# Kernel optimization log

Hardware: AMD Instinct MI355X
Metric: run time of the kernel (lower is better)

The kernel has to match this reference:

```python
import jax, jax.numpy as jnp
import numpy as np


def setup_inputs() -> dict:
    key = jax.random.key(0)
    k1, k2, k3, k4 = jax.random.split(key, 4)
    B, S, D, U = 4, 2048, 512, 256
    x = jax.random.normal(k1, (B, S, D), dtype=jnp.float32)
    scale = 1.0 / np.sqrt(D)  # ~glorot magnitude
    Wq = jax.random.normal(k2, (D, U), dtype=jnp.float32) * scale
    Wk = jax.random.normal(k3, (D, U), dtype=jnp.float32) * scale
    Wv = jax.random.normal(k4, (D, U), dtype=jnp.float32) * scale
    return {"x": x, "Wq": Wq, "Wk": Wk, "Wv": Wv}


def reference(x, Wq, Wk, Wv):
    # Single-head self-attention, NO 1/sqrt(d) scaling (faithful to source).
    q = jnp.einsum("bsd,du->bsu", x, Wq)
    k = jnp.einsum("bsd,du->bsu", x, Wk)
    v = jnp.einsum("bsd,du->bsu", x, Wv)
    scores = jnp.einsum("bsu,btu->bst", q, k)       # [B,S,S]
    attn = jax.nn.softmax(scores, axis=-1)
    out = jnp.einsum("bst,btu->bsu", attn, v)       # [B,S,U]
    return out
```

## Files before the change

kernel.cpp:

```cpp
#include <hip/hip_runtime.h>
#include <hip/hip_bf16.h>

typedef _Float16 f16;
typedef _Float16 f16x8 __attribute__((ext_vector_type(8)));
typedef _Float16 f16x4 __attribute__((ext_vector_type(4)));
typedef float    f32x4 __attribute__((ext_vector_type(4)));

#define DEV __device__ __forceinline__

DEV f16x8 load16(const void* p) {
  return __builtin_bit_cast(f16x8, *(const uint4*)p);
}
DEV f32x4 mfma(f16x8 a, f16x8 b, f32x4 c) {
  return __builtin_amdgcn_mfma_f32_16x16x32_f16(a, b, c, 0, 0, 0);
}
DEV void async_cp16(void* lds_dst, const void* gsrc) {
  __builtin_amdgcn_global_load_lds(
      (const __attribute__((address_space(1))) void*)gsrc,
      (__attribute__((address_space(3))) void*)lds_dst,
      16, 0, 0);
}
DEV int pk2(float a, float b) {
  return __builtin_bit_cast(int, __builtin_amdgcn_cvt_pkrtz(a, b));
}
DEV int bperm(int lane_times4, int v) {
  return __builtin_amdgcn_ds_bpermute(lane_times4, v);
}

__global__ __launch_bounds__(256) void k_cvt_x(const float4* __restrict__ x,
                                               f16x4* __restrict__ xf) {
  int gid = blockIdx.x * 256 + threadIdx.x;
  float4 v = x[gid];
  f16x4 h = {(f16)v.x, (f16)v.y, (f16)v.z, (f16)v.w};
  xf[gid] = h;
}

__global__ __launch_bounds__(256) void k_cvt_w(
    const float* __restrict__ Wq, const float* __restrict__ Wk, const float* __restrict__ Wv,
    f16* __restrict__ WqT, f16* __restrict__ WkT, f16* __restrict__ WvT) {
  int z = blockIdx.z;
  const float* W = (z == 0) ? Wq : (z == 1) ? Wk : Wv;
  f16* O = (z == 0) ? WqT : (z == 1) ? WkT : WvT;
  int t = blockIdx.x * 256 + threadIdx.x;
  int n = t & 255, k = t >> 8;
  O[n * 512 + k] = (f16)W[k * 256 + n];
}

__global__ __launch_bounds__(256, 3) void k_proj(
    const f16* __restrict__ xf,
    const f16* __restrict__ WqT, const f16* __restrict__ WkT, const f16* __restrict__ WvT,
    f16* __restrict__ Qf, f16* __restrict__ Kf, f16* __restrict__ Vt) {
  __shared__ __align__(16) unsigned char smem[49152];

  const int z = blockIdx.z;
  const f16* Bw = (z == 0) ? WqT : (z == 1) ? WkT : WvT;
  const int m0 = blockIdx.x * 128;
  const int n0 = blockIdx.y * 64;
  const int tid = threadIdx.x;
  const int w = tid >> 6, l = tid & 63;
  const int lr = l & 15, lg = l >> 4;
  const int wr = w >> 1, wc = w & 1;

  f32x4 acc[4][2] = {};

  const unsigned char* Ab = (const unsigned char*)xf;
  const unsigned char* Bb = (const unsigned char*)Bw;

  auto STAGE = [&](int kt, int bufo) {
    const int k0b = kt * 128;
#pragma unroll
    for (int ii = 0; ii < 4; ++ii) {
      int c = w * 4 + ii;
      int row = c * 8 + (l >> 3);
      async_cp16(smem + bufo + c * 1024,
                 Ab + (size_t)(m0 + row) * 1024 + k0b + (((l & 7) * 16) ^ ((l >> 3) << 4)));
    }
#pragma unroll
    for (int ii = 0; ii < 2; ++ii) {
      int c = w * 2 + ii;
      int row = c * 8 + (l >> 3);
      async_cp16(smem + bufo + 16384 + c * 1024,
                 Bb + (size_t)(n0 + row) * 1024 + k0b + (((l & 7) * 16) ^ ((l >> 3) << 4)));
    }
  };

  STAGE(0, 0);
  __syncthreads();

  for (int kt = 0; kt < 8; ++kt) {
    const int cur = (kt & 1) * 24576;
    if (kt < 7) STAGE(kt + 1, cur ^ 24576);
    const unsigned char* ldsA = smem + cur;
    const unsigned char* ldsB = smem + cur + 16384;
#pragma unroll
    for (int ks = 0; ks < 2; ++ks) {
      f16x8 af[4], bf[2];
      const int colb = ks * 64 + lg * 16;
#pragma unroll
      for (int mb = 0; mb < 4; ++mb) {
        int row = wr * 64 + mb * 16 + lr;
        af[mb] = load16(ldsA + row * 128 + (colb ^ ((row & 7) << 4)));
      }
#pragma unroll
      for (int nb = 0; nb < 2; ++nb) {
        int row = wc * 32 + nb * 16 + lr;
        bf[nb] = load16(ldsB + row * 128 + (colb ^ ((row & 7) << 4)));
      }
      if (z != 2) {
#pragma unroll
        for (int mb = 0; mb < 4; ++mb)
#pragma unroll
          for (int nb = 0; nb < 2; ++nb)
            acc[mb][nb] = mfma(af[mb], bf[nb], acc[mb][nb]);
      } else {
#pragma unroll
        for (int mb = 0; mb < 4; ++mb)
#pragma unroll
          for (int nb = 0; nb < 2; ++nb)
            acc[mb][nb] = mfma(bf[nb], af[mb], acc[mb][nb]);
      }
    }
    __syncthreads();
  }

  if (z != 2) {
    f16* O = (z == 0) ? Qf : Kf;
#pragma unroll
    for (int mb = 0; mb < 4; ++mb)
#pragma unroll
      for (int nb = 0; nb < 2; ++nb)
#pragma unroll
        for (int j = 0; j < 4; ++j) {
          int row = m0 + wr * 64 + mb * 16 + lg * 4 + j;
          int col = n0 + wc * 32 + nb * 16 + lr;
          O[(size_t)row * 256 + col] = (f16)acc[mb][nb][j];
        }
  } else {
    const int bb = m0 >> 11;
    const int tl0 = m0 & 2047;
#pragma unroll
    for (int mb = 0; mb < 4; ++mb)
#pragma unroll
      for (int nb = 0; nb < 2; ++nb)
#pragma unroll
        for (int j = 0; j < 4; ++j) {
          int u  = n0 + wc * 32 + nb * 16 + lg * 4 + j;
          int tg = tl0 + wr * 64 + mb * 16 + lr;
          Vt[((size_t)bb * 256 + u) * 2048 + tg] = (f16)acc[mb][nb][j];
        }
  }
}

__global__ __launch_bounds__(256, 2) void k_attn(
    const f16* __restrict__ Qf, const f16* __restrict__ Kf, const f16* __restrict__ Vt,
    f16* __restrict__ pO, float* __restrict__ pm, float* __restrict__ pl) {
  __shared__ __align__(16) unsigned char smem[65536];

  const int phys = blockIdx.x;
  const int idx  = (phys & 7) * 64 + (phys >> 3);
  const int chunk = idx >> 5, qt = idx & 31;
  const int b = chunk >> 2, qq = chunk & 3;
  const int q0 = qt * 64;
  const int tbase = qq * 512;

  const int tid = threadIdx.x, w = tid >> 6, l = tid & 63;
  const int lr = l & 15, lg = l >> 4;

  f16x8 qh[8];
  {
    const f16* qrow = Qf + (size_t)(b * 2048 + q0 + w * 16 + lr) * 256;
#pragma unroll
    for (int ks = 0; ks < 8; ++ks) qh[ks] = load16(qrow + ks * 32 + lg * 8);
  }

  f32x4 acc[16] = {};
  float mrun = -__builtin_inff(), lrun = 0.f;

  const unsigned char* Kb = (const unsigned char*)Kf + (size_t)b * 2048 * 512;
  const unsigned char* Vb = (const unsigned char*)Vt + (size_t)b * 256 * 4096;

  auto STAGE = [&](int it, int bufo) {
    const int t0 = tbase + it * 32;
#pragma unroll
    for (int ii = 0; ii < 8; ++ii) {
      int s = w * 8 + ii;
      if (s < 16) {
        int row = s * 2 + (l >> 5);
        async_cp16(smem + bufo + s * 1024,
                   Kb + (size_t)(t0 + row) * 512 + (((l & 31) * 16) ^ ((row & 7) << 4)));
      } else {
        int c = s - 16;
        int row = c * 16 + (l >> 2);
        async_cp16(smem + bufo + 16384 + c * 1024,
                   Vb + (size_t)row * 4096 + t0 * 2 + (((l & 3) * 16) ^ (((row >> 1) & 3) << 4)));
      }
    }
  };

  STAGE(0, 0);
  __syncthreads();

  for (int it = 0; it < 16; ++it) {
    const int cur = (it & 1) << 15;
    if (it < 15) STAGE(it + 1, cur ^ 32768);
    const unsigned char* ldsK = smem + cur;
    const unsigned char* ldsV = smem + cur + 16384;

    f32x4 s0 = {}, s1 = {};
    const int sw = (lr & 7) << 4;
#pragma unroll
    for (int ks = 0; ks < 8; ++ks) {
      const int colb = ks * 64 + lg * 16;
      f16x8 k0 = load16(ldsK + lr * 512 + (colb ^ sw));
      f16x8 k1 = load16(ldsK + (16 + lr) * 512 + (colb ^ sw));
      s0 = mfma(k0, qh[ks], s0);
      s1 = mfma(k1, qh[ks], s1);
    }

    float mt = fmaxf(fmaxf(fmaxf(s0[0], s0[1]), fmaxf(s0[2], s0[3])),
                     fmaxf(fmaxf(s1[0], s1[1]), fmaxf(s1[2], s1[3])));
    mt = fmaxf(mt, __shfl_xor(mt, 16, 64));
    mt = fmaxf(mt, __shfl_xor(mt, 32, 64));
    const bool need = !__all(mt <= mrun + 5.f);
    float al = 1.f;
    if (need) {
      float mn = fmaxf(mrun, mt);
      al = __expf(mrun - mn);
      mrun = mn;
    }
    float p0[4], p1[4];
#pragma unroll
    for (int j = 0; j < 4; ++j) {
      p0[j] = __expf(s0[j] - mrun);
      p1[j] = __expf(s1[j] - mrun);
    }
    float rs = (p0[0] + p0[1]) + (p0[2] + p0[3]) + (p1[0] + p1[1]) + (p1[2] + p1[3]);
    rs += __shfl_xor(rs, 16, 64);
    rs += __shfl_xor(rs, 32, 64);
    lrun = al * lrun + rs;

    if (need) {
      float alj[4];
#pragma unroll
      for (int j = 0; j < 4; ++j)
        alj[j] = __builtin_bit_cast(float, bperm((lg * 4 + j) * 4, __builtin_bit_cast(int, al)));
#pragma unroll
      for (int nb = 0; nb < 16; ++nb) {
        f32x4 a = acc[nb];
        a[0] *= alj[0]; a[1] *= alj[1]; a[2] *= alj[2]; a[3] *= alj[3];
        acc[nb] = a;
      }
    }

    int a0 = pk2(p0[0], p0[1]), a1 = pk2(p0[2], p0[3]);
    int b0 = pk2(p1[0], p1[1]), b1 = pk2(p1[2], p1[3]);
    const int srcA = (lr + ((lg & 1) ? 32 : 0)) * 4;
    const int srcB = srcA + 64;
    int ta0 = bperm(srcA, a0), ta1 = bperm(srcA, a1);
    int tb0 = bperm(srcA, b0), tb1 = bperm(srcA, b1);
    int ua0 = bperm(srcB, a0), ua1 = bperm(srcB, a1);
    int ub0 = bperm(srcB, b0), ub1 = bperm(srcB, b1);
    const bool useb = lg >= 2;
    int d0 = useb ? tb0 : ta0;
    int d1 = useb ? tb1 : ta1;
    int d2 = useb ? ub0 : ua0;
    int d3 = useb ? ub1 : ua1;
    int4 dv = {d0, d1, d2, d3};
    f16x8 pa = __builtin_bit_cast(f16x8, dv);

#pragma unroll
    for (int nb = 0; nb < 16; ++nb) {
      int ru = nb * 16 + lr;
      f16x8 vf = load16(ldsV + ru * 64 + ((lg * 16) ^ (((ru >> 1) & 3) << 4)));
      acc[nb] = mfma(pa, vf, acc[nb]);
    }

    __syncthreads();
  }

  const size_t prow = (size_t)idx * 64 + w * 16;
#pragma unroll
  for (int nb = 0; nb < 16; ++nb)
#pragma unroll
    for (int j = 0; j < 4; ++j)
      pO[(prow + lg * 4 + j) * 256 + nb * 16 + lr] = (f16)acc[nb][j];
  if (l < 16) {
    pm[prow + lr] = mrun;
    pl[prow + lr] = lrun;
  }
}

__global__ __launch_bounds__(256) void k_combine(
    const f16* __restrict__ pO, const float* __restrict__ pm, const float* __restrict__ pl,
    float* __restrict__ out) {
  int gid = blockIdx.x * 256 + threadIdx.x;
  int gr = gid >> 6, uq = gid & 63;
  int b = gr >> 11, r = gr & 2047;
  int qt = r >> 6, rr = r & 63;
  float mv[4];
#pragma unroll
  for (int q = 0; q < 4; ++q)
    mv[q] = pm[(size_t)((b * 4 + q) * 32 + qt) * 64 + rr];
  float m = fmaxf(fmaxf(mv[0], mv[1]), fmaxf(mv[2], mv[3]));
  float lsum = 0.f, wq[4];
#pragma unroll
  for (int q = 0; q < 4; ++q) {
    wq[q] = __expf(mv[q] - m);
    lsum += wq[q] * pl[(size_t)((b * 4 + q) * 32 + qt) * 64 + rr];
  }
  f32x4 o = {};
#pragma unroll
  for (int q = 0; q < 4; ++q) {
    const f16x4 hv = *(const f16x4*)(pO + ((size_t)((b * 4 + q) * 32 + qt) * 64 + rr) * 256 + uq * 4);
    f32x4 v = {(float)hv[0], (float)hv[1], (float)hv[2], (float)hv[3]};
    o += v * wq[q];
  }
  f32x4 res = o * (1.0f / lsum);
  *(f32x4*)(out + (size_t)gr * 256 + uq * 4) = res;
}

extern "C" void kernel_launch(void* const* d_in, const int* in_sizes, int n_in,
                              void* d_out, int out_size, void* d_ws, size_t ws_size,
                              hipStream_t stream) {
  const float* x  = (const float*)d_in[0];
  const float* Wq = (const float*)d_in[1];
  const float* Wk = (const float*)d_in[2];
  const float* Wv = (const float*)d_in[3];
  float* out = (float*)d_out;

  unsigned char* ws = (unsigned char*)d_ws;
  f16*   xf  = (f16*)(ws + 0);
  f16*   WqT = (f16*)(ws + 8388608);
  f16*   WkT = (f16*)(ws + 8650752);
  f16*   WvT = (f16*)(ws + 8912896);
  f16*   Qf  = (f16*)(ws + 9175040);
  f16*   Kf  = (f16*)(ws + 13369344);
  f16*   Vt  = (f16*)(ws + 17563648);
  f16*   pO  = (f16*)(ws + 21757952);
  float* pm  = (float*)(ws + 38535168);
  float* pl  = (float*)(ws + 38666240);

  k_cvt_x<<<4096, 256, 0, stream>>>((const float4*)x, (f16x4*)xf);
  k_cvt_w<<<dim3(512, 1, 3), 256, 0, stream>>>(Wq, Wk, Wv, WqT, WkT, WvT);
  k_proj<<<dim3(64, 4, 3), 256, 0, stream>>>(xf, WqT, WkT, WvT, Qf, Kf, Vt);
  k_attn<<<512, 256, 0, stream>>>(Qf, Kf, Vt, pO, pm, pl);
  k_combine<<<2048, 256, 0, stream>>>(pO, pm, pl, out);
}
```

Baseline: 127.6 us.

## Fuse QKV projections per block, double attention key splits, read V from global

The projection kernel now computes Q, K and V together for a 64-row tile, sharing one staged x tile across the three weight matrices instead of launching a separate z-slice for each. The attention kernel splits the key range into 8 chunks instead of 4, giving 1024 blocks with half the LDS so more blocks fit per CU. V is no longer staged in LDS; its fragments are loaded straight from global memory inside the loop. The combine kernel merges 8 partials instead of 4, which means more partial output traffic, and the uncached V loads may add latency.

```diff
diff --git a/kernel.cpp b/kernel.cpp
--- a/kernel.cpp
+++ b/kernel.cpp
@@ -46,41 +46,42 @@
   O[n * 512 + k] = (f16)W[k * 256 + n];
 }
 
-__global__ __launch_bounds__(256, 3) void k_proj(
+__global__ __launch_bounds__(256, 2) void k_proj(
     const f16* __restrict__ xf,
     const f16* __restrict__ WqT, const f16* __restrict__ WkT, const f16* __restrict__ WvT,
     f16* __restrict__ Qf, f16* __restrict__ Kf, f16* __restrict__ Vt) {
-  __shared__ __align__(16) unsigned char smem[49152];
-
-  const int z = blockIdx.z;
-  const f16* Bw = (z == 0) ? WqT : (z == 1) ? WkT : WvT;
-  const int m0 = blockIdx.x * 128;
+  __shared__ __align__(16) unsigned char smem[65536];
+
+  const int m0 = blockIdx.x * 64;
   const int n0 = blockIdx.y * 64;
   const int tid = threadIdx.x;
   const int w = tid >> 6, l = tid & 63;
   const int lr = l & 15, lg = l >> 4;
-  const int wr = w >> 1, wc = w & 1;
-
-  f32x4 acc[4][2] = {};
+
+  f32x4 acc[3][4] = {};
 
   const unsigned char* Ab = (const unsigned char*)xf;
-  const unsigned char* Bb = (const unsigned char*)Bw;
+  const unsigned char* Wb[3] = {(const unsigned char*)WqT, (const unsigned char*)WkT,
+                                (const unsigned char*)WvT};
 
   auto STAGE = [&](int kt, int bufo) {
     const int k0b = kt * 128;
-#pragma unroll
-    for (int ii = 0; ii < 4; ++ii) {
-      int c = w * 4 + ii;
-      int row = c * 8 + (l >> 3);
-      async_cp16(smem + bufo + c * 1024,
-                 Ab + (size_t)(m0 + row) * 1024 + k0b + (((l & 7) * 16) ^ ((l >> 3) << 4)));
-    }
-#pragma unroll
-    for (int ii = 0; ii < 2; ++ii) {
-      int c = w * 2 + ii;
-      int row = c * 8 + (l >> 3);
-      async_cp16(smem + bufo + 16384 + c * 1024,
-                 Bb + (size_t)(n0 + row) * 1024 + k0b + (((l & 7) * 16) ^ ((l >> 3) << 4)));
+    const int swz = ((l & 7) * 16) ^ ((l >> 3) << 4);
+    if (w == 0) {
+#pragma unroll
+      for (int c = 0; c < 8; ++c) {
+        int row = c * 8 + (l >> 3);
+        async_cp16(smem + bufo + c * 1024,
+                   Ab + (size_t)(m0 + row) * 1024 + k0b + swz);
+      }
+    } else {
+      const unsigned char* Bg = Wb[w - 1];
+#pragma unroll
+      for (int c = 0; c < 8; ++c) {
+        int row = c * 8 + (l >> 3);
+        async_cp16(smem + bufo + 8192 + (w - 1) * 8192 + c * 1024,
+                   Bg + (size_t)(n0 + row) * 1024 + k0b + swz);
+      }
     }
   };
 
@@ -88,80 +89,69 @@
   __syncthreads();
 
   for (int kt = 0; kt < 8; ++kt) {
-    const int cur = (kt & 1) * 24576;
-    if (kt < 7) STAGE(kt + 1, cur ^ 24576);
+    const int cur = (kt & 1) << 15;
+    if (kt < 7) STAGE(kt + 1, cur ^ 32768);
     const unsigned char* ldsA = smem + cur;
-    const unsigned char* ldsB = smem + cur + 16384;
+    const unsigned char* ldsB = smem + cur + 8192;
 #pragma unroll
     for (int ks = 0; ks < 2; ++ks) {
-      f16x8 af[4], bf[2];
       const int colb = ks * 64 + lg * 16;
+      f16x8 af[4], bf[3];
 #pragma unroll
       for (int mb = 0; mb < 4; ++mb) {
-        int row = wr * 64 + mb * 16 + lr;
+        int row = mb * 16 + lr;
         af[mb] = load16(ldsA + row * 128 + (colb ^ ((row & 7) << 4)));
       }
-#pragma unroll
-      for (int nb = 0; nb < 2; ++nb) {
-        int row = wc * 32 + nb * 16 + lr;
-        bf[nb] = load16(ldsB + row * 128 + (colb ^ ((row & 7) << 4)));
-      }
-      if (z != 2) {
-#pragma unroll
-        for (int mb = 0; mb < 4; ++mb)
-#pragma unroll
-          for (int nb = 0; nb < 2; ++nb)
-            acc[mb][nb] = mfma(af[mb], bf[nb], acc[mb][nb]);
-      } else {
-#pragma unroll
-        for (int mb = 0; mb < 4; ++mb)
-#pragma unroll
-          for (int nb = 0; nb < 2; ++nb)
-            acc[mb][nb] = mfma(bf[nb], af[mb], acc[mb][nb]);
+      {
+        int row = w * 16 + lr;
+        int off = row * 128 + (colb ^ ((row & 7) << 4));
+#pragma unroll
+        for (int g = 0; g < 3; ++g) bf[g] = load16(ldsB + g * 8192 + off);
+      }
+#pragma unroll
+      for (int mb = 0; mb < 4; ++mb) {
+        acc[0][mb] = mfma(af[mb], bf[0], acc[0][mb]);
+        acc[1][mb] = mfma(af[mb], bf[1], acc[1][mb]);
+        acc[2][mb] = mfma(bf[2], af[mb], acc[2][mb]);
       }
     }
     __syncthreads();
   }
 
-  if (z != 2) {
-    f16* O = (z == 0) ? Qf : Kf;
-#pragma unroll
-    for (int mb = 0; mb < 4; ++mb)
-#pragma unroll
-      for (int nb = 0; nb < 2; ++nb)
-#pragma unroll
-        for (int j = 0; j < 4; ++j) {
-          int row = m0 + wr * 64 + mb * 16 + lg * 4 + j;
-          int col = n0 + wc * 32 + nb * 16 + lr;
-          O[(size_t)row * 256 + col] = (f16)acc[mb][nb][j];
-        }
-  } else {
+#pragma unroll
+  for (int mb = 0; mb < 4; ++mb)
+#pragma unroll
+    for (int j = 0; j < 4; ++j) {
+      int row = m0 + mb * 16 + lg * 4 + j;
+      int col = n0 + w * 16 + lr;
+      Qf[(size_t)row * 256 + col] = (f16)acc[0][mb][j];
+      Kf[(size_t)row * 256 + col] = (f16)acc[1][mb][j];
+    }
+  {
     const int bb = m0 >> 11;
     const int tl0 = m0 & 2047;
 #pragma unroll
     for (int mb = 0; mb < 4; ++mb)
 #pragma unroll
-      for (int nb = 0; nb < 2; ++nb)
-#pragma unroll
-        for (int j = 0; j < 4; ++j) {
-          int u  = n0 + wc * 32 + nb * 16 + lg * 4 + j;
-          int tg = tl0 + wr * 64 + mb * 16 + lr;
-          Vt[((size_t)bb * 256 + u) * 2048 + tg] = (f16)acc[mb][nb][j];
-        }
-  }
-}
-
-__global__ __launch_bounds__(256, 2) void k_attn(
+      for (int j = 0; j < 4; ++j) {
+        int u  = n0 + w * 16 + lg * 4 + j;
+        int tg = tl0 + mb * 16 + lr;
+        Vt[((size_t)bb * 256 + u) * 2048 + tg] = (f16)acc[2][mb][j];
+      }
+  }
+}
+
+__global__ __launch_bounds__(256, 4) void k_attn(
     const f16* __restrict__ Qf, const f16* __restrict__ Kf, const f16* __restrict__ Vt,
     f16* __restrict__ pO, float* __restrict__ pm, float* __restrict__ pl) {
-  __shared__ __align__(16) unsigned char smem[65536];
+  __shared__ __align__(16) unsigned char smem[32768];
 
   const int phys = blockIdx.x;
-  const int idx  = (phys & 7) * 64 + (phys >> 3);
+  const int idx  = (phys & 7) * 128 + (phys >> 3);
   const int chunk = idx >> 5, qt = idx & 31;
-  const int b = chunk >> 2, qq = chunk & 3;
+  const int b = chunk >> 3, qq = chunk & 7;
   const int q0 = qt * 64;
-  const int tbase = qq * 512;
+  const int tbase = qq * 256;
 
   const int tid = threadIdx.x, w = tid >> 6, l = tid & 63;
   const int lr = l & 15, lg = l >> 4;
@@ -182,29 +172,23 @@
   auto STAGE = [&](int it, int bufo) {
     const int t0 = tbase + it * 32;
 #pragma unroll
-    for (int ii = 0; ii < 8; ++ii) {
-      int s = w * 8 + ii;
-      if (s < 16) {
-        int row = s * 2 + (l >> 5);
-        async_cp16(smem + bufo + s * 1024,
-                   Kb + (size_t)(t0 + row) * 512 + (((l & 31) * 16) ^ ((row & 7) << 4)));
-      } else {
-        int c = s - 16;
-        int row = c * 16 + (l >> 2);
-        async_cp16(smem + bufo + 16384 + c * 1024,
-                   Vb + (size_t)row * 4096 + t0 * 2 + (((l & 3) * 16) ^ (((row >> 1) & 3) << 4)));
-      }
+    for (int ii = 0; ii < 4; ++ii) {
+      int c = w * 4 + ii;
+      int row = c * 2 + (l >> 5);
+      async_cp16(smem + bufo + c * 1024,
+                 Kb + (size_t)(t0 + row) * 512 + (((l & 31) * 16) ^ ((row & 7) << 4)));
     }
   };
 
   STAGE(0, 0);
   __syncthreads();
 
-  for (int it = 0; it < 16; ++it) {
-    const int cur = (it & 1) << 15;
-    if (it < 15) STAGE(it + 1, cur ^ 32768);
+  for (int it = 0; it < 8; ++it) {
+    const int cur = (it & 1) << 14;
+    if (it < 7) STAGE(it + 1, cur ^ 16384);
     const unsigned char* ldsK = smem + cur;
-    const unsigned char* ldsV = smem + cur + 16384;
+    const int t0 = tbase + it * 32;
+    const unsigned char* Vit = Vb + (size_t)t0 * 2 + lg * 16;
 
     f32x4 s0 = {}, s1 = {};
     const int sw = (lr & 7) << 4;
@@ -271,7 +255,7 @@
 #pragma unroll
     for (int nb = 0; nb < 16; ++nb) {
       int ru = nb * 16 + lr;
-      f16x8 vf = load16(ldsV + ru * 64 + ((lg * 16) ^ (((ru >> 1) & 3) << 4)));
+      f16x8 vf = load16(Vit + (size_t)ru * 4096);
       acc[nb] = mfma(pa, vf, acc[nb]);
     }
 
@@ -297,21 +281,22 @@
   int gr = gid >> 6, uq = gid & 63;
   int b = gr >> 11, r = gr & 2047;
   int qt = r >> 6, rr = r & 63;
-  float mv[4];
-#pragma unroll
-  for (int q = 0; q < 4; ++q)
-    mv[q] = pm[(size_t)((b * 4 + q) * 32 + qt) * 64 + rr];
-  float m = fmaxf(fmaxf(mv[0], mv[1]), fmaxf(mv[2], mv[3]));
-  float lsum = 0.f, wq[4];
-#pragma unroll
-  for (int q = 0; q < 4; ++q) {
+  float mv[8];
+#pragma unroll
+  for (int q = 0; q < 8; ++q)
+    mv[q] = pm[(size_t)((b * 8 + q) * 32 + qt) * 64 + rr];
+  float m = fmaxf(fmaxf(fmaxf(mv[0], mv[1]), fmaxf(mv[2], mv[3])),
+                  fmaxf(fmaxf(mv[4], mv[5]), fmaxf(mv[6], mv[7])));
+  float lsum = 0.f, wq[8];
+#pragma unroll
+  for (int q = 0; q < 8; ++q) {
     wq[q] = __expf(mv[q] - m);
-    lsum += wq[q] * pl[(size_t)((b * 4 + q) * 32 + qt) * 64 + rr];
+    lsum += wq[q] * pl[(size_t)((b * 8 + q) * 32 + qt) * 64 + rr];
   }
   f32x4 o = {};
 #pragma unroll
-  for (int q = 0; q < 4; ++q) {
-    const f16x4 hv = *(const f16x4*)(pO + ((size_t)((b * 4 + q) * 32 + qt) * 64 + rr) * 256 + uq * 4);
+  for (int q = 0; q < 8; ++q) {
+    const f16x4 hv = *(const f16x4*)(pO + ((size_t)((b * 8 + q) * 32 + qt) * 64 + rr) * 256 + uq * 4);
     f32x4 v = {(float)hv[0], (float)hv[1], (float)hv[2], (float)hv[3]};
     o += v * wq[q];
   }
@@ -337,12 +322,12 @@
   f16*   Kf  = (f16*)(ws + 13369344);
   f16*   Vt  = (f16*)(ws + 17563648);
   f16*   pO  = (f16*)(ws + 21757952);
-  float* pm  = (float*)(ws + 38535168);
-  float* pl  = (float*)(ws + 38666240);
+  float* pm  = (float*)(ws + 55312384);
+  float* pl  = (float*)(ws + 55574528);
 
   k_cvt_x<<<4096, 256, 0, stream>>>((const float4*)x, (f16x4*)xf);
   k_cvt_w<<<dim3(512, 1, 3), 256, 0, stream>>>(Wq, Wk, Wv, WqT, WkT, WvT);
-  k_proj<<<dim3(64, 4, 3), 256, 0, stream>>>(xf, WqT, WkT, WvT, Qf, Kf, Vt);
-  k_attn<<<512, 256, 0, stream>>>(Qf, Kf, Vt, pO, pm, pl);
+  k_proj<<<dim3(128, 4), 256, 0, stream>>>(xf, WqT, WkT, WvT, Qf, Kf, Vt);
+  k_attn<<<1024, 256, 0, stream>>>(Qf, Kf, Vt, pO, pm, pl);
   k_combine<<<2048, 256, 0, stream>>>(pO, pm, pl, out);
 }
```

Measured after the change: 189.9 us. +48.8%, slower.
